# Performance work log

Measured on AMD Instinct MI355X. Metric: run time of the kernel, lower is better.

The kernel has to match this reference:

```python
import jax, jax.numpy as jnp
import numpy as np

B, T, D = 32, 512, 384
MAX_DUR = 4                 # durations drawn from [0, MAX_DUR]
MAX_FRAMES = T * MAX_DUR    # static padded output length (>= any per-batch total)
PAD_VALUE = 0.0


def setup_inputs() -> dict:
    key = jax.random.key(0)
    k1, k2 = jax.random.split(key)
    xs = jax.random.normal(k1, (B, T, D), dtype=jnp.float32)
    ds = jax.random.randint(k2, (B, T), 0, MAX_DUR + 1).astype(jnp.int64)
    return {"xs": xs, "ds": ds}


def reference(xs, ds):
    # Faithful LengthRegulator.forward with alpha == 1.0 (default):
    # expand each phoneme embedding by its duration, pad sequences to a
    # common length with pad_value. Instead of a per-sample Python loop +
    # repeat_interleave, we compute cumulative durations and map every
    # output frame t to its source phoneme via searchsorted (gather).
    ds = ds.astype(jnp.int32)
    # ESPnet safeguard: rows with all-zero durations are filled with 1s.
    row_all_zero = (ds.sum(axis=1) == 0)[:, None]          # (B, 1)
    ds = jnp.where(row_all_zero, 1, ds)

    cum = jnp.cumsum(ds, axis=1)                            # (B, T)
    totals = cum[:, -1]                                     # (B,)
    t = jnp.arange(MAX_FRAMES, dtype=jnp.int32)             # (MAX_FRAMES,)
    # frame t belongs to phoneme i where cum[i-1] <= t < cum[i]
    idx = jax.vmap(lambda c: jnp.searchsorted(c, t, side='right'))(cum)  # (B, MAX_FRAMES)
    idx = jnp.clip(idx, 0, T - 1)
    valid = t[None, :] < totals[:, None]                    # (B, MAX_FRAMES)

    out = jnp.take_along_axis(xs, idx[:, :, None], axis=1)  # (B, MAX_FRAMES, D)
    return jnp.where(valid[:, :, None], out, jnp.asarray(PAD_VALUE, xs.dtype))
```

## Files before the change

kernel.cpp:

```cpp
#include <hip/hip_runtime.h>

#define NB 32
#define NT 512
#define ND 384
#define NC (ND / 4)
#define NFRAMES 2048

__global__ __launch_bounds__(NT) void lr_index_kernel(const int* __restrict__ ds,
                                                      int* __restrict__ idx) {
    __shared__ int cum[NT];
    const int b = blockIdx.x;
    const int t = threadIdx.x;

    int d = ds[b * NT + t];
    cum[t] = d;
    __syncthreads();

    #pragma unroll
    for (int off = 1; off < NT; off <<= 1) {
        int v = (t >= off) ? cum[t - off] : 0;
        __syncthreads();
        cum[t] += v;
        __syncthreads();
    }

    const int total = cum[NT - 1];
    if (total == 0) {
        d = 1;
        cum[t] = t + 1;
    }

    int* idx_row = idx + b * NFRAMES;
    #pragma unroll
    for (int k = 0; k < NFRAMES / NT; ++k)
        idx_row[t + k * NT] = -1;
    __syncthreads();

    const int end = cum[t];
    for (int p = end - d; p < end; ++p)
        idx_row[p] = t;
}

__global__ __launch_bounds__(256) void lr_gather_kernel(const float4* __restrict__ xs,
                                                        const int* __restrict__ idx,
                                                        float4* __restrict__ out) {
    const int n = NB * NFRAMES * NC;
    const int stride = gridDim.x * blockDim.x;
    for (int i = blockIdx.x * blockDim.x + threadIdx.x; i < n; i += stride) {
        const int frame = i / NC;
        const int c = i - frame * NC;
        const int b = frame >> 11;
        const int j = idx[frame];
        float4 v;
        if (j >= 0) {
            v = xs[(b * NT + j) * NC + c];
        } else {
            v = make_float4(0.f, 0.f, 0.f, 0.f);
        }
        out[i] = v;
    }
}

extern "C" void kernel_launch(void* const* d_in, const int* in_sizes, int n_in,
                              void* d_out, int out_size, void* d_ws, size_t ws_size,
                              hipStream_t stream) {
    const float* xs = (const float*)d_in[0];
    const int*   ds = (const int*)d_in[1];
    float* out = (float*)d_out;
    int* idx = (int*)d_ws;

    lr_index_kernel<<<NB, NT, 0, stream>>>(ds, idx);

    const int n = NB * NFRAMES * NC;
    const int block = 256;
    int grid = 2048;
    (void)n; (void)in_sizes; (void)n_in; (void)out_size; (void)ws_size;
    lr_gather_kernel<<<grid, block, 0, stream>>>((const float4*)xs, idx, (float4*)out);
}
```

Baseline: 128.1 us.

## Fuse index computation and gather into one kernel with per-slice binary search

Replaces the two-kernel scheme (prefix sum writing a global index map, then a grid-stride gather) with a single kernel. Each block covers one slice of 128 frames for one batch, redoes the prefix scan in shared memory, finds source phonemes by binary search into a shared index table, and then copies rows. This drops the second launch and the global round trip of the index array. The cost is that every slice block repeats the 512-element scan, and the grid is only 512 blocks of 512 threads.

```diff
diff --git a/kernel.cpp b/kernel.cpp
--- a/kernel.cpp
+++ b/kernel.cpp
@@ -2,20 +2,23 @@
 
 #define NB 32
 #define NT 512
-#define ND 384
-#define NC (ND / 4)
+#define NC 96
 #define NFRAMES 2048
+#define SLICES 16
+#define FPS (NFRAMES / SLICES)
+#define ITERS (FPS * NC / NT)
 
-__global__ __launch_bounds__(NT) void lr_index_kernel(const int* __restrict__ ds,
-                                                      int* __restrict__ idx) {
+__global__ __launch_bounds__(NT) void lr_fused_kernel(const int* __restrict__ ds,
+                                                      const float4* __restrict__ xs,
+                                                      float4* __restrict__ out) {
     __shared__ int cum[NT];
-    const int b = blockIdx.x;
+    __shared__ int sidx[FPS];
     const int t = threadIdx.x;
+    const int slice = blockIdx.x;
+    const int b = blockIdx.y;
 
-    int d = ds[b * NT + t];
-    cum[t] = d;
+    cum[t] = ds[b * NT + t];
     __syncthreads();
-
     #pragma unroll
     for (int off = 1; off < NT; off <<= 1) {
         int v = (t >= off) ? cum[t - off] : 0;
@@ -24,40 +27,38 @@
         __syncthreads();
     }
 
-    const int total = cum[NT - 1];
+    int total = cum[NT - 1];
     if (total == 0) {
-        d = 1;
         cum[t] = t + 1;
+        total = NT;
     }
-
-    int* idx_row = idx + b * NFRAMES;
-    #pragma unroll
-    for (int k = 0; k < NFRAMES / NT; ++k)
-        idx_row[t + k * NT] = -1;
     __syncthreads();
 
-    const int end = cum[t];
-    for (int p = end - d; p < end; ++p)
-        idx_row[p] = t;
-}
+    if (t < FPS) {
+        const int p = slice * FPS + t;
+        int j = -1;
+        if (p < total) {
+            int lo = 0, hi = NT;
+            while (lo < hi) {
+                const int mid = (lo + hi) >> 1;
+                if (cum[mid] > p) hi = mid; else lo = mid + 1;
+            }
+            j = lo;
+        }
+        sidx[t] = j;
+    }
+    __syncthreads();
 
-__global__ __launch_bounds__(256) void lr_gather_kernel(const float4* __restrict__ xs,
-                                                        const int* __restrict__ idx,
-                                                        float4* __restrict__ out) {
-    const int n = NB * NFRAMES * NC;
-    const int stride = gridDim.x * blockDim.x;
-    for (int i = blockIdx.x * blockDim.x + threadIdx.x; i < n; i += stride) {
-        const int frame = i / NC;
-        const int c = i - frame * NC;
-        const int b = frame >> 11;
-        const int j = idx[frame];
-        float4 v;
-        if (j >= 0) {
-            v = xs[(b * NT + j) * NC + c];
-        } else {
-            v = make_float4(0.f, 0.f, 0.f, 0.f);
-        }
-        out[i] = v;
+    const float4* __restrict__ xrow = xs + (size_t)b * NT * NC;
+    float4* __restrict__ orow = out + ((size_t)b * NFRAMES + (size_t)slice * FPS) * NC;
+    const float4 z = make_float4(0.f, 0.f, 0.f, 0.f);
+    #pragma unroll
+    for (int it = 0; it < ITERS; ++it) {
+        const int e = it * NT + t;
+        const int fr = e / NC;
+        const int c = e - fr * NC;
+        const int j = sidx[fr];
+        orow[e] = (j >= 0) ? xrow[j * NC + c] : z;
     }
 }
 
@@ -67,13 +68,8 @@
     const float* xs = (const float*)d_in[0];
     const int*   ds = (const int*)d_in[1];
     float* out = (float*)d_out;
-    int* idx = (int*)d_ws;
+    (void)in_sizes; (void)n_in; (void)out_size; (void)d_ws; (void)ws_size;
 
-    lr_index_kernel<<<NB, NT, 0, stream>>>(ds, idx);
-
-    const int n = NB * NFRAMES * NC;
-    const int block = 256;
-    int grid = 2048;
-    (void)n; (void)in_sizes; (void)n_in; (void)out_size; (void)ws_size;
-    lr_gather_kernel<<<grid, block, 0, stream>>>((const float4*)xs, idx, (float4*)out);
+    dim3 grid(SLICES, NB);
+    lr_fused_kernel<<<grid, NT, 0, stream>>>(ds, (const float4*)xs, (float4*)out);
 }
```

Result: slower. 132.1 us (+3.2%).
